# Performance work log

Measured on AMD Instinct MI355X. Metric: run time of the kernel, lower is better.

The kernel has to match this reference:

```python
import jax, jax.numpy as jnp
import numpy as np

B, N, IN_DIM, OUT_DIM, HEADS = 4, 2048, 128, 32, 8
NEG_SLOPE = 0.2


def setup_inputs() -> dict:
    key = jax.random.key(0)
    k_x, k_adj, k_w, k_as, k_ad = jax.random.split(key, 5)
    x = jax.random.normal(k_x, (B, N, IN_DIM), dtype=jnp.float32)
    adj = jax.random.randint(k_adj, (B, N, N), 0, 2).astype(jnp.float32)
    # xavier_uniform bounds
    lim_w = float(np.sqrt(6.0 / (IN_DIM + OUT_DIM)))
    lim_a = float(np.sqrt(6.0 / (OUT_DIM + 1)))
    W = jax.random.uniform(k_w, (HEADS, IN_DIM, OUT_DIM), dtype=jnp.float32, minval=-lim_w, maxval=lim_w)
    a_src = jax.random.uniform(k_as, (HEADS, OUT_DIM), dtype=jnp.float32, minval=-lim_a, maxval=lim_a)
    a_dst = jax.random.uniform(k_ad, (HEADS, OUT_DIM), dtype=jnp.float32, minval=-lim_a, maxval=lim_a)
    return {"x": x, "adj": adj, "W": W, "a_src": a_src, "a_dst": a_dst}


def reference(x, adj, W, a_src, a_dst):
    # Wh: [B,H,N,O]
    Wh = jnp.einsum('bnf,hfo->bhno', x, W)
    alpha_src = jnp.einsum('bhno,ho->bhn', Wh, a_src)  # [B,H,N]
    alpha_dst = jnp.einsum('bhno,ho->bhn', Wh, a_dst)  # [B,H,N]
    # additive scores e[b,h,i,j] = alpha_src[b,h,i] + alpha_dst[b,h,j]
    e = alpha_src[..., :, None] + alpha_dst[..., None, :]
    e = jnp.where(e >= 0, e, NEG_SLOPE * e)  # leaky_relu(0.2)
    n = adj.shape[-1]
    eye = jnp.eye(n, dtype=adj.dtype)
    mask = (adj + eye[None] > 0)[:, None, :, :]  # [B,1,N,N]
    e = jnp.where(mask, e, -jnp.inf)
    attn = jax.nn.softmax(e, axis=-1)  # every row has self-loop -> finite
    out = jnp.einsum('bhij,bhjo->bhio', attn, Wh)  # [B,H,N,O]
    b = x.shape[0]
    out = jnp.transpose(out, (0, 2, 1, 3)).reshape(b, n, HEADS * OUT_DIM)
    return jax.nn.relu(out)
```

## Files before the change

kernel.cpp:

```cpp
#include <hip/hip_runtime.h>
#include <math.h>

#define BB 4
#define NSZ 2048
#define FDIM 128
#define ODIM 32
#define HH 8

typedef short short8 __attribute__((ext_vector_type(8)));
typedef float f32x4 __attribute__((ext_vector_type(4)));

#define WS_EAP  0
#define WS_EBP  131072
#define WS_ADJB 262144
#define WS_WHF  786432

__device__ __forceinline__ unsigned bfbits(float f) {
    unsigned u = __builtin_bit_cast(unsigned, f);
    return u + 0x7fffu + ((u >> 16) & 1u);
}
__device__ __forceinline__ unsigned bfpack(float a, float b) {
    return __builtin_amdgcn_perm(bfbits(b), bfbits(a), 0x07060302);
}

__global__ __launch_bounds__(256) void k_prep(const float* __restrict__ x,
                                              const float* __restrict__ adj,
                                              const float* __restrict__ W,
                                              const float* __restrict__ a_src,
                                              const float* __restrict__ a_dst,
                                              unsigned* __restrict__ adjb,
                                              int4* __restrict__ whf,
                                              float2* __restrict__ eap,
                                              float2* __restrict__ ebp) {
    __shared__ float wsl[FDIM * 33];
    __shared__ unsigned short wlds[64][33];
    int t = threadIdx.x;

    if (blockIdx.x < 16384) {
        int g = blockIdx.x * 256 + t;
        int l = g & 7;
        int word = g >> 3;
        int wk = word & 63;
        int row = word >> 6;
        int i = row & (NSZ - 1);
        const float4 v = *(const float4*)&adj[(size_t)row * NSZ + wk * 32 + l * 4];
        unsigned m = 0;
        if (v.x > 0.f) m |= 1u << (l * 4 + 0);
        if (v.y > 0.f) m |= 1u << (l * 4 + 1);
        if (v.z > 0.f) m |= 1u << (l * 4 + 2);
        if (v.w > 0.f) m |= 1u << (l * 4 + 3);
        m |= (unsigned)__shfl_xor((int)m, 1);
        m |= (unsigned)__shfl_xor((int)m, 2);
        m |= (unsigned)__shfl_xor((int)m, 4);
        if (l == 0) {
            int jb = i - wk * 32;
            if (jb >= 0 && jb < 32) m |= 1u << jb;
            adjb[word] = m;
        }
        return;
    }

    int bidx = blockIdx.x - 16384;
    int b = bidx >> 8;
    int h = (bidx >> 5) & 7;
    int nt = bidx & 31;
    int n0 = nt * 64;
    int w = t >> 6, lane = t & 63;
    int col = lane & 15, quad = lane >> 4;

#pragma unroll
    for (int m = 0; m < 16; m++) {
        int idx = t + m * 256;
        wsl[(idx >> 5) * 33 + (idx & 31)] = W[(size_t)h * (FDIM * ODIM) + idx];
    }

    const float* xp = x + ((size_t)(b * NSZ) + n0 + w * 16 + col) * FDIM + quad * 8;
    int4 afr[4];
#pragma unroll
    for (int kt = 0; kt < 4; kt++) {
        float4 xa = *(const float4*)(xp + kt * 32);
        float4 xb = *(const float4*)(xp + kt * 32 + 4);
        afr[kt] = make_int4((int)bfpack(xa.x, xa.y), (int)bfpack(xa.z, xa.w),
                            (int)bfpack(xb.x, xb.y), (int)bfpack(xb.z, xb.w));
    }
    __syncthreads();

    f32x4 alo = {0.f, 0.f, 0.f, 0.f};
    f32x4 ahi = {0.f, 0.f, 0.f, 0.f};
#pragma unroll
    for (int kt = 0; kt < 4; kt++) {
        short8 a8 = __builtin_bit_cast(short8, afr[kt]);
#pragma unroll
        for (int ot = 0; ot < 2; ot++) {
            unsigned d[4];
#pragma unroll
            for (int jp = 0; jp < 4; jp++) {
                float lo = wsl[(kt * 32 + quad * 8 + 2 * jp) * 33 + ot * 16 + col];
                float hi = wsl[(kt * 32 + quad * 8 + 2 * jp + 1) * 33 + ot * 16 + col];
                d[jp] = bfpack(lo, hi);
            }
            int4 bf = make_int4((int)d[0], (int)d[1], (int)d[2], (int)d[3]);
            if (ot == 0)
                alo = __builtin_amdgcn_mfma_f32_16x16x32_bf16(a8,
                        __builtin_bit_cast(short8, bf), alo, 0, 0, 0);
            else
                ahi = __builtin_amdgcn_mfma_f32_16x16x32_bf16(a8,
                        __builtin_bit_cast(short8, bf), ahi, 0, 0, 0);
        }
    }

    float as0 = a_src[h * ODIM + col], as1 = a_src[h * ODIM + 16 + col];
    float ad0 = a_dst[h * ODIM + col], ad1 = a_dst[h * ODIM + 16 + col];
#pragma unroll
    for (int r = 0; r < 4; r++) {
        float pa = alo[r] * as0 + ahi[r] * as1;
        float pb = alo[r] * ad0 + ahi[r] * ad1;
#pragma unroll
        for (int mk = 1; mk <= 8; mk <<= 1) {
            pa += __shfl_xor(pa, mk);
            pb += __shfl_xor(pb, mk);
        }
        if (col == 0) {
            size_t idx = (size_t)(b * HH + h) * NSZ + n0 + w * 16 + quad * 4 + r;
            eap[idx] = make_float2(__expf(pa - 8.f), __expf(0.2f * pa - 8.f));
            ebp[idx] = make_float2(__expf(pb - 8.f), __expf(0.2f * pb - 8.f));
        }
    }

#pragma unroll
    for (int r = 0; r < 4; r++) {
        wlds[w * 16 + quad * 4 + r][col]      = (unsigned short)(bfbits(alo[r]) >> 16);
        wlds[w * 16 + quad * 4 + r][col + 16] = (unsigned short)(bfbits(ahi[r]) >> 16);
    }
    __syncthreads();
    int jl = w >> 1, ot = w & 1;
    unsigned d[4];
#pragma unroll
    for (int jp = 0; jp < 4; jp++) {
        unsigned lo = wlds[jl * 32 + quad * 8 + 2 * jp][ot * 16 + col];
        unsigned hi = wlds[jl * 32 + quad * 8 + 2 * jp + 1][ot * 16 + col];
        d[jp] = (hi << 16) | lo;
    }
    int fragid = ((b * HH + h) * 64 + nt * 2 + jl) * 2 + ot;
    whf[(size_t)fragid * 64 + lane] = make_int4((int)d[0], (int)d[1], (int)d[2], (int)d[3]);
}

__device__ __forceinline__ int4 pfrag(float eaa, float eab, const float4& l0,
                                      const float4& l1, const float4& l2,
                                      const float4& l3, unsigned word, int shb) {
    float p0 = fmaxf(eaa * l0.x, eab * l0.y);
    float p1 = fmaxf(eaa * l0.z, eab * l0.w);
    float p2 = fmaxf(eaa * l1.x, eab * l1.y);
    float p3 = fmaxf(eaa * l1.z, eab * l1.w);
    float p4 = fmaxf(eaa * l2.x, eab * l2.y);
    float p5 = fmaxf(eaa * l2.z, eab * l2.w);
    float p6 = fmaxf(eaa * l3.x, eab * l3.y);
    float p7 = fmaxf(eaa * l3.z, eab * l3.w);
    unsigned d0 = __builtin_amdgcn_perm(__builtin_bit_cast(unsigned, p1),
                                        __builtin_bit_cast(unsigned, p0), 0x07060302);
    unsigned d1 = __builtin_amdgcn_perm(__builtin_bit_cast(unsigned, p3),
                                        __builtin_bit_cast(unsigned, p2), 0x07060302);
    unsigned d2 = __builtin_amdgcn_perm(__builtin_bit_cast(unsigned, p5),
                                        __builtin_bit_cast(unsigned, p4), 0x07060302);
    unsigned d3 = __builtin_amdgcn_perm(__builtin_bit_cast(unsigned, p7),
                                        __builtin_bit_cast(unsigned, p6), 0x07060302);
    unsigned mk[4];
#pragma unroll
    for (int k = 0; k < 4; k++) {
        int s0 = ((int)(word << (shb - 2 * k))) >> 31;
        int s1 = ((int)(word << (shb - 2 * k - 1))) >> 31;
        mk[k] = __builtin_amdgcn_perm((unsigned)s1, (unsigned)s0, 0x07060302);
    }
    return make_int4((int)(d0 & mk[0]), (int)(d1 & mk[1]),
                     (int)(d2 & mk[2]), (int)(d3 & mk[3]));
}

__global__ __launch_bounds__(256, 4) void k_gat(const int4* __restrict__ whf,
                                                const float2* __restrict__ eap,
                                                const float2* __restrict__ ebp,
                                                const unsigned* __restrict__ adjb,
                                                float* __restrict__ out) {
    __shared__ float sbuf[6144];

    int t = threadIdx.x;
    int u = blockIdx.x;
    int unit = (u & 7) * 128 + (u >> 3);
    int b = unit >> 8;
    int h = (unit >> 5) & 7;
    int i0 = (unit & 31) * 64;
    int wave = t >> 6, lane = t & 63;
    int col = lane & 15, quad = lane >> 4, qsh = quad * 8;
    int shb = 31 - qsh;
    size_t bh = (size_t)(b * HH + h);

    const float4* ebg = (const float4*)(ebp + bh * NSZ);
#pragma unroll
    for (int k = 0; k < 4; k++) ((float4*)sbuf)[t + k * 256] = ebg[t + k * 256];

    float2 ea[4];
    const uint4* mp[4];
#pragma unroll
    for (int f = 0; f < 4; f++) {
        ea[f] = eap[bh * NSZ + i0 + f * 16 + col];
        mp[f] = (const uint4*)(adjb + ((size_t)(b * NSZ) + i0 + f * 16 + col) * 64) + wave * 4;
    }
    const int4* bfp = whf + bh * 8192 + lane;

    f32x4 ac[4][3];
#pragma unroll
    for (int f = 0; f < 4; f++)
#pragma unroll
        for (int c = 0; c < 3; c++) ac[f][c] = (f32x4){0.f, 0.f, 0.f, 0.f};
    const int4 onesv = make_int4(0x3F803F80, 0x3F803F80, 0x3F803F80, 0x3F803F80);
    short8 bones = __builtin_bit_cast(short8, onesv);

    __syncthreads();

    for (int jt4 = 0; jt4 < 4; jt4++) {
        uint4 mw[4];
#pragma unroll
        for (int f = 0; f < 4; f++) mw[f] = mp[f][jt4];
#pragma unroll
        for (int q = 0; q < 4; q++) {
            int jt = wave * 16 + jt4 * 4 + q;
            const float4* el = (const float4*)&sbuf[(jt * 32 + qsh) * 2];
            float4 l0 = el[0], l1 = el[1], l2 = el[2], l3 = el[3];
            int4 blo = bfp[jt * 128];
            int4 bhi = bfp[jt * 128 + 64];
            short8 b0 = __builtin_bit_cast(short8, blo);
            short8 b1 = __builtin_bit_cast(short8, bhi);
            unsigned wq[4] = {mw[0].x, mw[1].x, mw[2].x, mw[3].x};
            if (q == 1) { wq[0] = mw[0].y; wq[1] = mw[1].y; wq[2] = mw[2].y; wq[3] = mw[3].y; }
            if (q == 2) { wq[0] = mw[0].z; wq[1] = mw[1].z; wq[2] = mw[2].z; wq[3] = mw[3].z; }
            if (q == 3) { wq[0] = mw[0].w; wq[1] = mw[1].w; wq[2] = mw[2].w; wq[3] = mw[3].w; }
#pragma unroll
            for (int f = 0; f < 4; f++) {
                int4 fr = pfrag(ea[f].x, ea[f].y, l0, l1, l2, l3, wq[f], shb);
                short8 a8 = __builtin_bit_cast(short8, fr);
                ac[f][0] = __builtin_amdgcn_mfma_f32_16x16x32_bf16(a8, b0, ac[f][0], 0, 0, 0);
                ac[f][1] = __builtin_amdgcn_mfma_f32_16x16x32_bf16(a8, b1, ac[f][1], 0, 0, 0);
                ac[f][2] = __builtin_amdgcn_mfma_f32_16x16x32_bf16(a8, bones, ac[f][2], 0, 0, 0);
            }
        }
    }

    f32x4* reg0 = (f32x4*)&sbuf[0];
    f32x4* reg1 = (f32x4*)&sbuf[3072];
    __syncthreads();
    if (wave >= 2) {
        f32x4* rg = (wave == 2) ? reg0 : reg1;
#pragma unroll
        for (int f = 0; f < 4; f++)
#pragma unroll
            for (int c = 0; c < 3; c++) rg[(f * 3 + c) * 64 + lane] = ac[f][c];
    }
    __syncthreads();
    if (wave < 2) {
        f32x4* rg = (wave == 0) ? reg0 : reg1;
#pragma unroll
        for (int f = 0; f < 4; f++)
#pragma unroll
            for (int c = 0; c < 3; c++) {
                f32x4 v = rg[(f * 3 + c) * 64 + lane];
#pragma unroll
                for (int r = 0; r < 4; r++) ac[f][c][r] += v[r];
            }
    }
    __syncthreads();
    if (wave == 1) {
#pragma unroll
        for (int f = 0; f < 4; f++)
#pragma unroll
            for (int c = 0; c < 3; c++) reg0[(f * 3 + c) * 64 + lane] = ac[f][c];
    }
    __syncthreads();
    if (wave != 0) return;
#pragma unroll
    for (int f = 0; f < 4; f++)
#pragma unroll
        for (int c = 0; c < 3; c++) {
            f32x4 v = reg0[(f * 3 + c) * 64 + lane];
#pragma unroll
            for (int r = 0; r < 4; r++) ac[f][c][r] += v[r];
        }

    float* op = out + ((size_t)(b * NSZ) + i0) * (HH * ODIM) + h * ODIM + col;
#pragma unroll
    for (int f = 0; f < 4; f++)
#pragma unroll
        for (int r = 0; r < 4; r++) {
            int row = f * 16 + quad * 4 + r;
            float inv = 1.0f / ac[f][2][r];
            op[(size_t)row * (HH * ODIM)]      = fmaxf(ac[f][0][r] * inv, 0.f);
            op[(size_t)row * (HH * ODIM) + 16] = fmaxf(ac[f][1][r] * inv, 0.f);
        }
}

extern "C" void kernel_launch(void* const* d_in, const int* in_sizes, int n_in,
                              void* d_out, int out_size, void* d_ws, size_t ws_size,
                              hipStream_t stream) {
    const float* x     = (const float*)d_in[0];
    const float* adj   = (const float*)d_in[1];
    const float* W     = (const float*)d_in[2];
    const float* a_src = (const float*)d_in[3];
    const float* a_dst = (const float*)d_in[4];
    float* out = (float*)d_out;

    float* ws = (float*)d_ws;
    float2* eap    = (float2*)(ws + WS_EAP);
    float2* ebp    = (float2*)(ws + WS_EBP);
    unsigned* adjb = (unsigned*)(ws + WS_ADJB);
    int4* whf      = (int4*)(ws + WS_WHF);

    k_prep<<<dim3(16384 + 1024), dim3(256), 0, stream>>>(x, adj, W, a_src, a_dst,
                                                         adjb, whf, eap, ebp);
    k_gat<<<dim3(BB * HH * (NSZ / 64)), dim3(256), 0, stream>>>(whf, eap, ebp, adjb, out);
}
```

Baseline: 146.2 us.

## Pack dst exponentials as bf16 pairs, software-pipeline loads, flatten wave reduction

```diff
diff --git a/kernel.cpp b/kernel.cpp
--- a/kernel.cpp
+++ b/kernel.cpp
@@ -11,9 +11,9 @@
 typedef float f32x4 __attribute__((ext_vector_type(4)));
 
 #define WS_EAP  0
-#define WS_EBP  131072
-#define WS_ADJB 262144
-#define WS_WHF  786432
+#define WS_EBPK 131072
+#define WS_ADJB 196608
+#define WS_WHF  720896
 
 __device__ __forceinline__ unsigned bfbits(float f) {
     unsigned u = __builtin_bit_cast(unsigned, f);
@@ -31,7 +31,7 @@
                                               unsigned* __restrict__ adjb,
                                               int4* __restrict__ whf,
                                               float2* __restrict__ eap,
-                                              float2* __restrict__ ebp) {
+                                              unsigned* __restrict__ ebpk) {
     __shared__ float wsl[FDIM * 33];
     __shared__ unsigned short wlds[64][33];
     int t = threadIdx.x;
@@ -123,7 +123,9 @@
         if (col == 0) {
             size_t idx = (size_t)(b * HH + h) * NSZ + n0 + w * 16 + quad * 4 + r;
             eap[idx] = make_float2(__expf(pa - 8.f), __expf(0.2f * pa - 8.f));
-            ebp[idx] = make_float2(__expf(pb - 8.f), __expf(0.2f * pb - 8.f));
+            float e1 = __expf(pb - 8.f);
+            float e2 = __expf(0.2f * pb - 8.f);
+            ebpk[idx] = (bfbits(e2) & 0xffff0000u) | (bfbits(e1) >> 16);
         }
     }
 
@@ -145,42 +147,35 @@
     whf[(size_t)fragid * 64 + lane] = make_int4((int)d[0], (int)d[1], (int)d[2], (int)d[3]);
 }
 
-__device__ __forceinline__ int4 pfrag(float eaa, float eab, const float4& l0,
-                                      const float4& l1, const float4& l2,
-                                      const float4& l3, unsigned word, int shb) {
-    float p0 = fmaxf(eaa * l0.x, eab * l0.y);
-    float p1 = fmaxf(eaa * l0.z, eab * l0.w);
-    float p2 = fmaxf(eaa * l1.x, eab * l1.y);
-    float p3 = fmaxf(eaa * l1.z, eab * l1.w);
-    float p4 = fmaxf(eaa * l2.x, eab * l2.y);
-    float p5 = fmaxf(eaa * l2.z, eab * l2.w);
-    float p6 = fmaxf(eaa * l3.x, eab * l3.y);
-    float p7 = fmaxf(eaa * l3.z, eab * l3.w);
-    unsigned d0 = __builtin_amdgcn_perm(__builtin_bit_cast(unsigned, p1),
-                                        __builtin_bit_cast(unsigned, p0), 0x07060302);
-    unsigned d1 = __builtin_amdgcn_perm(__builtin_bit_cast(unsigned, p3),
-                                        __builtin_bit_cast(unsigned, p2), 0x07060302);
-    unsigned d2 = __builtin_amdgcn_perm(__builtin_bit_cast(unsigned, p5),
-                                        __builtin_bit_cast(unsigned, p4), 0x07060302);
-    unsigned d3 = __builtin_amdgcn_perm(__builtin_bit_cast(unsigned, p7),
-                                        __builtin_bit_cast(unsigned, p6), 0x07060302);
-    unsigned mk[4];
+__device__ __forceinline__ int4 pfrag_pk(float eaa, float eab,
+                                         const int4& ca, const int4& cb, unsigned w) {
+    unsigned pd[8] = {(unsigned)ca.x, (unsigned)ca.y, (unsigned)ca.z, (unsigned)ca.w,
+                      (unsigned)cb.x, (unsigned)cb.y, (unsigned)cb.z, (unsigned)cb.w};
+    unsigned dw[4];
 #pragma unroll
     for (int k = 0; k < 4; k++) {
-        int s0 = ((int)(word << (shb - 2 * k))) >> 31;
-        int s1 = ((int)(word << (shb - 2 * k - 1))) >> 31;
-        mk[k] = __builtin_amdgcn_perm((unsigned)s1, (unsigned)s0, 0x07060302);
-    }
-    return make_int4((int)(d0 & mk[0]), (int)(d1 & mk[1]),
-                     (int)(d2 & mk[2]), (int)(d3 & mk[3]));
+        float e0  = __builtin_bit_cast(float, pd[2 * k] << 16);
+        float e0b = __builtin_bit_cast(float, pd[2 * k] & 0xffff0000u);
+        float e1  = __builtin_bit_cast(float, pd[2 * k + 1] << 16);
+        float e1b = __builtin_bit_cast(float, pd[2 * k + 1] & 0xffff0000u);
+        float pL = fmaxf(eaa * e0, eab * e0b);
+        float pH = fmaxf(eaa * e1, eab * e1b);
+        unsigned d = __builtin_amdgcn_perm(__builtin_bit_cast(unsigned, pH),
+                                           __builtin_bit_cast(unsigned, pL), 0x07060302);
+        int s0 = ((int)(w << (31 - 2 * k))) >> 31;
+        int s1 = ((int)(w << (30 - 2 * k))) >> 31;
+        unsigned mk = __builtin_amdgcn_perm((unsigned)s1, (unsigned)s0, 0x07060302);
+        dw[k] = d & mk;
+    }
+    return make_int4((int)dw[0], (int)dw[1], (int)dw[2], (int)dw[3]);
 }
 
 __global__ __launch_bounds__(256, 4) void k_gat(const int4* __restrict__ whf,
                                                 const float2* __restrict__ eap,
-                                                const float2* __restrict__ ebp,
+                                                const unsigned* __restrict__ ebpk,
                                                 const unsigned* __restrict__ adjb,
                                                 float* __restrict__ out) {
-    __shared__ float sbuf[6144];
+    __shared__ float sbuf[9216];
 
     int t = threadIdx.x;
     int u = blockIdx.x;
@@ -190,19 +185,19 @@
     int i0 = (unit & 31) * 64;
     int wave = t >> 6, lane = t & 63;
     int col = lane & 15, quad = lane >> 4, qsh = quad * 8;
-    int shb = 31 - qsh;
     size_t bh = (size_t)(b * HH + h);
 
-    const float4* ebg = (const float4*)(ebp + bh * NSZ);
-#pragma unroll
-    for (int k = 0; k < 4; k++) ((float4*)sbuf)[t + k * 256] = ebg[t + k * 256];
+    unsigned* sbu = (unsigned*)sbuf;
+    const uint4* ebg = (const uint4*)(ebpk + bh * NSZ);
+    ((uint4*)sbu)[t] = ebg[t];
+    ((uint4*)sbu)[t + 256] = ebg[t + 256];
 
     float2 ea[4];
-    const uint4* mp[4];
+    const unsigned* mr[4];
 #pragma unroll
     for (int f = 0; f < 4; f++) {
         ea[f] = eap[bh * NSZ + i0 + f * 16 + col];
-        mp[f] = (const uint4*)(adjb + ((size_t)(b * NSZ) + i0 + f * 16 + col) * 64) + wave * 4;
+        mr[f] = adjb + ((size_t)(b * NSZ) + i0 + f * 16 + col) * 64;
     }
     const int4* bfp = whf + bh * 8192 + lane;
 
@@ -216,47 +211,50 @@
 
     __syncthreads();
 
-    for (int jt4 = 0; jt4 < 4; jt4++) {
-        uint4 mw[4];
-#pragma unroll
-        for (int f = 0; f < 4; f++) mw[f] = mp[f][jt4];
-#pragma unroll
-        for (int q = 0; q < 4; q++) {
-            int jt = wave * 16 + jt4 * 4 + q;
-            const float4* el = (const float4*)&sbuf[(jt * 32 + qsh) * 2];
-            float4 l0 = el[0], l1 = el[1], l2 = el[2], l3 = el[3];
-            int4 blo = bfp[jt * 128];
-            int4 bhi = bfp[jt * 128 + 64];
-            short8 b0 = __builtin_bit_cast(short8, blo);
-            short8 b1 = __builtin_bit_cast(short8, bhi);
-            unsigned wq[4] = {mw[0].x, mw[1].x, mw[2].x, mw[3].x};
-            if (q == 1) { wq[0] = mw[0].y; wq[1] = mw[1].y; wq[2] = mw[2].y; wq[3] = mw[3].y; }
-            if (q == 2) { wq[0] = mw[0].z; wq[1] = mw[1].z; wq[2] = mw[2].z; wq[3] = mw[3].z; }
-            if (q == 3) { wq[0] = mw[0].w; wq[1] = mw[1].w; wq[2] = mw[2].w; wq[3] = mw[3].w; }
-#pragma unroll
-            for (int f = 0; f < 4; f++) {
-                int4 fr = pfrag(ea[f].x, ea[f].y, l0, l1, l2, l3, wq[f], shb);
-                short8 a8 = __builtin_bit_cast(short8, fr);
-                ac[f][0] = __builtin_amdgcn_mfma_f32_16x16x32_bf16(a8, b0, ac[f][0], 0, 0, 0);
-                ac[f][1] = __builtin_amdgcn_mfma_f32_16x16x32_bf16(a8, b1, ac[f][1], 0, 0, 0);
-                ac[f][2] = __builtin_amdgcn_mfma_f32_16x16x32_bf16(a8, bones, ac[f][2], 0, 0, 0);
-            }
-        }
-    }
-
-    f32x4* reg0 = (f32x4*)&sbuf[0];
-    f32x4* reg1 = (f32x4*)&sbuf[3072];
-    __syncthreads();
-    if (wave >= 2) {
-        f32x4* rg = (wave == 2) ? reg0 : reg1;
+    int jt0 = wave * 16;
+    int4 c_e0 = ((const int4*)sbu)[jt0 * 8 + quad * 2];
+    int4 c_e1 = ((const int4*)sbu)[jt0 * 8 + quad * 2 + 1];
+    int4 c_b0 = bfp[jt0 * 128];
+    int4 c_b1 = bfp[jt0 * 128 + 64];
+    unsigned c_w0 = mr[0][jt0], c_w1 = mr[1][jt0], c_w2 = mr[2][jt0], c_w3 = mr[3][jt0];
+
+    for (int s = 0; s < 16; s++) {
+        int jn = jt0 + ((s + 1) & 15);
+        int4 n_e0 = ((const int4*)sbu)[jn * 8 + quad * 2];
+        int4 n_e1 = ((const int4*)sbu)[jn * 8 + quad * 2 + 1];
+        int4 n_b0 = bfp[jn * 128];
+        int4 n_b1 = bfp[jn * 128 + 64];
+        unsigned n_w0 = mr[0][jn], n_w1 = mr[1][jn], n_w2 = mr[2][jn], n_w3 = mr[3][jn];
+
+        short8 b0 = __builtin_bit_cast(short8, c_b0);
+        short8 b1 = __builtin_bit_cast(short8, c_b1);
+        unsigned cw[4] = {c_w0, c_w1, c_w2, c_w3};
+#pragma unroll
+        for (int f = 0; f < 4; f++) {
+            int4 fr = pfrag_pk(ea[f].x, ea[f].y, c_e0, c_e1, cw[f] >> qsh);
+            short8 a8 = __builtin_bit_cast(short8, fr);
+            ac[f][0] = __builtin_amdgcn_mfma_f32_16x16x32_bf16(a8, b0, ac[f][0], 0, 0, 0);
+            ac[f][1] = __builtin_amdgcn_mfma_f32_16x16x32_bf16(a8, b1, ac[f][1], 0, 0, 0);
+            ac[f][2] = __builtin_amdgcn_mfma_f32_16x16x32_bf16(a8, bones, ac[f][2], 0, 0, 0);
+        }
+
+        c_e0 = n_e0; c_e1 = n_e1; c_b0 = n_b0; c_b1 = n_b1;
+        c_w0 = n_w0; c_w1 = n_w1; c_w2 = n_w2; c_w3 = n_w3;
+    }
+
+    __syncthreads();
+    if (wave != 0) {
+        f32x4* rg = (f32x4*)&sbuf[(wave - 1) * 3072];
 #pragma unroll
         for (int f = 0; f < 4; f++)
 #pragma unroll
             for (int c = 0; c < 3; c++) rg[(f * 3 + c) * 64 + lane] = ac[f][c];
     }
     __syncthreads();
-    if (wave < 2) {
-        f32x4* rg = (wave == 0) ? reg0 : reg1;
+    if (wave != 0) return;
+#pragma unroll
+    for (int wv = 0; wv < 3; wv++) {
+        f32x4* rg = (f32x4*)&sbuf[wv * 3072];
 #pragma unroll
         for (int f = 0; f < 4; f++)
 #pragma unroll
@@ -266,23 +264,6 @@
                 for (int r = 0; r < 4; r++) ac[f][c][r] += v[r];
             }
     }
-    __syncthreads();
-    if (wave == 1) {
-#pragma unroll
-        for (int f = 0; f < 4; f++)
-#pragma unroll
-            for (int c = 0; c < 3; c++) reg0[(f * 3 + c) * 64 + lane] = ac[f][c];
-    }
-    __syncthreads();
-    if (wave != 0) return;
-#pragma unroll
-    for (int f = 0; f < 4; f++)
-#pragma unroll
-        for (int c = 0; c < 3; c++) {
-            f32x4 v = reg0[(f * 3 + c) * 64 + lane];
-#pragma unroll
-            for (int r = 0; r < 4; r++) ac[f][c][r] += v[r];
-        }
 
     float* op = out + ((size_t)(b * NSZ) + i0) * (HH * ODIM) + h * ODIM + col;
 #pragma unroll
@@ -308,11 +289,11 @@
 
     float* ws = (float*)d_ws;
     float2* eap    = (float2*)(ws + WS_EAP);
-    float2* ebp    = (float2*)(ws + WS_EBP);
+    unsigned* ebpk = (unsigned*)(ws + WS_EBPK);
     unsigned* adjb = (unsigned*)(ws + WS_ADJB);
     int4* whf      = (int4*)(ws + WS_WHF);
 
     k_prep<<<dim3(16384 + 1024), dim3(256), 0, stream>>>(x, adj, W, a_src, a_dst,
-                                                         adjb, whf, eap, ebp);
-    k_gat<<<dim3(BB * HH * (NSZ / 64)), dim3(256), 0, stream>>>(whf, eap, ebp, adjb, out);
-}
+                                                         adjb, whf, eap, ebpk);
+    k_gat<<<dim3(BB * HH * (NSZ / 64)), dim3(256), 0, stream>>>(whf, eap, ebpk, adjb, out);
+}
```

Result: no change. 148.1 us (+1.3%).

## Use one-wave blocks over 16 rows with transposed adjacency bitmask layout

Applied to the files above, without the earlier changes.

```diff
diff --git a/kernel.cpp b/kernel.cpp
--- a/kernel.cpp
+++ b/kernel.cpp
@@ -43,6 +43,7 @@
         int wk = word & 63;
         int row = word >> 6;
         int i = row & (NSZ - 1);
+        int b = row >> 11;
         const float4 v = *(const float4*)&adj[(size_t)row * NSZ + wk * 32 + l * 4];
         unsigned m = 0;
         if (v.x > 0.f) m |= 1u << (l * 4 + 0);
@@ -55,7 +56,7 @@
         if (l == 0) {
             int jb = i - wk * 32;
             if (jb >= 0 && jb < 32) m |= 1u << jb;
-            adjb[word] = m;
+            adjb[((size_t)b * 64 + wk) * NSZ + i] = m;
         }
         return;
     }
@@ -147,7 +148,7 @@
 
 __device__ __forceinline__ int4 pfrag(float eaa, float eab, const float4& l0,
                                       const float4& l1, const float4& l2,
-                                      const float4& l3, unsigned word, int shb) {
+                                      const float4& l3, unsigned w) {
     float p0 = fmaxf(eaa * l0.x, eab * l0.y);
     float p1 = fmaxf(eaa * l0.z, eab * l0.w);
     float p2 = fmaxf(eaa * l1.x, eab * l1.y);
@@ -167,133 +168,62 @@
     unsigned mk[4];
 #pragma unroll
     for (int k = 0; k < 4; k++) {
-        int s0 = ((int)(word << (shb - 2 * k))) >> 31;
-        int s1 = ((int)(word << (shb - 2 * k - 1))) >> 31;
+        int s0 = ((int)(w << (31 - 2 * k))) >> 31;
+        int s1 = ((int)(w << (30 - 2 * k))) >> 31;
         mk[k] = __builtin_amdgcn_perm((unsigned)s1, (unsigned)s0, 0x07060302);
     }
     return make_int4((int)(d0 & mk[0]), (int)(d1 & mk[1]),
                      (int)(d2 & mk[2]), (int)(d3 & mk[3]));
 }
 
-__global__ __launch_bounds__(256, 4) void k_gat(const int4* __restrict__ whf,
-                                                const float2* __restrict__ eap,
-                                                const float2* __restrict__ ebp,
-                                                const unsigned* __restrict__ adjb,
-                                                float* __restrict__ out) {
-    __shared__ float sbuf[6144];
-
-    int t = threadIdx.x;
-    int u = blockIdx.x;
-    int unit = (u & 7) * 128 + (u >> 3);
-    int b = unit >> 8;
-    int h = (unit >> 5) & 7;
-    int i0 = (unit & 31) * 64;
-    int wave = t >> 6, lane = t & 63;
+__global__ __launch_bounds__(64, 8) void k_gat(const int4* __restrict__ whf,
+                                               const float2* __restrict__ eap,
+                                               const float2* __restrict__ ebp,
+                                               const unsigned* __restrict__ adjb,
+                                               float* __restrict__ out) {
+    int lane = threadIdx.x & 63;
+    int unit = blockIdx.x;
+    int i0 = (unit & 127) << 4;
+    int bh = unit >> 7;
+    int b = bh >> 3, h = bh & 7;
     int col = lane & 15, quad = lane >> 4, qsh = quad * 8;
-    int shb = 31 - qsh;
-    size_t bh = (size_t)(b * HH + h);
-
-    const float4* ebg = (const float4*)(ebp + bh * NSZ);
-#pragma unroll
-    for (int k = 0; k < 4; k++) ((float4*)sbuf)[t + k * 256] = ebg[t + k * 256];
-
-    float2 ea[4];
-    const uint4* mp[4];
-#pragma unroll
-    for (int f = 0; f < 4; f++) {
-        ea[f] = eap[bh * NSZ + i0 + f * 16 + col];
-        mp[f] = (const uint4*)(adjb + ((size_t)(b * NSZ) + i0 + f * 16 + col) * 64) + wave * 4;
-    }
-    const int4* bfp = whf + bh * 8192 + lane;
-
-    f32x4 ac[4][3];
-#pragma unroll
-    for (int f = 0; f < 4; f++)
-#pragma unroll
-        for (int c = 0; c < 3; c++) ac[f][c] = (f32x4){0.f, 0.f, 0.f, 0.f};
+
+    float2 ea = eap[(size_t)bh * NSZ + i0 + col];
+    const float4* eb4 = (const float4*)(ebp + (size_t)bh * NSZ) + quad * 4;
+    const unsigned* abp = adjb + (size_t)b * (64 * NSZ) + i0 + col;
+    const int4* bfp = whf + (size_t)bh * 8192 + lane;
+
+    f32x4 acc0 = {0.f, 0.f, 0.f, 0.f};
+    f32x4 acc1 = {0.f, 0.f, 0.f, 0.f};
+    f32x4 accd = {0.f, 0.f, 0.f, 0.f};
     const int4 onesv = make_int4(0x3F803F80, 0x3F803F80, 0x3F803F80, 0x3F803F80);
     short8 bones = __builtin_bit_cast(short8, onesv);
-
-    __syncthreads();
-
-    for (int jt4 = 0; jt4 < 4; jt4++) {
-        uint4 mw[4];
-#pragma unroll
-        for (int f = 0; f < 4; f++) mw[f] = mp[f][jt4];
-#pragma unroll
-        for (int q = 0; q < 4; q++) {
-            int jt = wave * 16 + jt4 * 4 + q;
-            const float4* el = (const float4*)&sbuf[(jt * 32 + qsh) * 2];
-            float4 l0 = el[0], l1 = el[1], l2 = el[2], l3 = el[3];
-            int4 blo = bfp[jt * 128];
-            int4 bhi = bfp[jt * 128 + 64];
-            short8 b0 = __builtin_bit_cast(short8, blo);
-            short8 b1 = __builtin_bit_cast(short8, bhi);
-            unsigned wq[4] = {mw[0].x, mw[1].x, mw[2].x, mw[3].x};
-            if (q == 1) { wq[0] = mw[0].y; wq[1] = mw[1].y; wq[2] = mw[2].y; wq[3] = mw[3].y; }
-            if (q == 2) { wq[0] = mw[0].z; wq[1] = mw[1].z; wq[2] = mw[2].z; wq[3] = mw[3].z; }
-            if (q == 3) { wq[0] = mw[0].w; wq[1] = mw[1].w; wq[2] = mw[2].w; wq[3] = mw[3].w; }
-#pragma unroll
-            for (int f = 0; f < 4; f++) {
-                int4 fr = pfrag(ea[f].x, ea[f].y, l0, l1, l2, l3, wq[f], shb);
-                short8 a8 = __builtin_bit_cast(short8, fr);
-                ac[f][0] = __builtin_amdgcn_mfma_f32_16x16x32_bf16(a8, b0, ac[f][0], 0, 0, 0);
-                ac[f][1] = __builtin_amdgcn_mfma_f32_16x16x32_bf16(a8, b1, ac[f][1], 0, 0, 0);
-                ac[f][2] = __builtin_amdgcn_mfma_f32_16x16x32_bf16(a8, bones, ac[f][2], 0, 0, 0);
-            }
-        }
-    }
-
-    f32x4* reg0 = (f32x4*)&sbuf[0];
-    f32x4* reg1 = (f32x4*)&sbuf[3072];
-    __syncthreads();
-    if (wave >= 2) {
-        f32x4* rg = (wave == 2) ? reg0 : reg1;
-#pragma unroll
-        for (int f = 0; f < 4; f++)
-#pragma unroll
-            for (int c = 0; c < 3; c++) rg[(f * 3 + c) * 64 + lane] = ac[f][c];
-    }
-    __syncthreads();
-    if (wave < 2) {
-        f32x4* rg = (wave == 0) ? reg0 : reg1;
-#pragma unroll
-        for (int f = 0; f < 4; f++)
-#pragma unroll
-            for (int c = 0; c < 3; c++) {
-                f32x4 v = rg[(f * 3 + c) * 64 + lane];
-#pragma unroll
-                for (int r = 0; r < 4; r++) ac[f][c][r] += v[r];
-            }
-    }
-    __syncthreads();
-    if (wave == 1) {
-#pragma unroll
-        for (int f = 0; f < 4; f++)
-#pragma unroll
-            for (int c = 0; c < 3; c++) reg0[(f * 3 + c) * 64 + lane] = ac[f][c];
-    }
-    __syncthreads();
-    if (wave != 0) return;
-#pragma unroll
-    for (int f = 0; f < 4; f++)
-#pragma unroll
-        for (int c = 0; c < 3; c++) {
-            f32x4 v = reg0[(f * 3 + c) * 64 + lane];
-#pragma unroll
-            for (int r = 0; r < 4; r++) ac[f][c][r] += v[r];
-        }
+    float eaa = ea.x, eab = ea.y;
+
+#pragma unroll 2
+    for (int jt = 0; jt < 64; jt++) {
+        unsigned w = abp[jt * NSZ] >> qsh;
+        float4 l0 = eb4[jt * 16 + 0];
+        float4 l1 = eb4[jt * 16 + 1];
+        float4 l2 = eb4[jt * 16 + 2];
+        float4 l3 = eb4[jt * 16 + 3];
+        int4 blo = bfp[jt * 128];
+        int4 bhi = bfp[jt * 128 + 64];
+        int4 fr = pfrag(eaa, eab, l0, l1, l2, l3, w);
+        short8 a8 = __builtin_bit_cast(short8, fr);
+        acc0 = __builtin_amdgcn_mfma_f32_16x16x32_bf16(a8, __builtin_bit_cast(short8, blo), acc0, 0, 0, 0);
+        acc1 = __builtin_amdgcn_mfma_f32_16x16x32_bf16(a8, __builtin_bit_cast(short8, bhi), acc1, 0, 0, 0);
+        accd = __builtin_amdgcn_mfma_f32_16x16x32_bf16(a8, bones, accd, 0, 0, 0);
+    }
 
     float* op = out + ((size_t)(b * NSZ) + i0) * (HH * ODIM) + h * ODIM + col;
 #pragma unroll
-    for (int f = 0; f < 4; f++)
-#pragma unroll
-        for (int r = 0; r < 4; r++) {
-            int row = f * 16 + quad * 4 + r;
-            float inv = 1.0f / ac[f][2][r];
-            op[(size_t)row * (HH * ODIM)]      = fmaxf(ac[f][0][r] * inv, 0.f);
-            op[(size_t)row * (HH * ODIM) + 16] = fmaxf(ac[f][1][r] * inv, 0.f);
-        }
+    for (int r = 0; r < 4; r++) {
+        int row = quad * 4 + r;
+        float inv = 1.0f / accd[r];
+        op[(size_t)row * (HH * ODIM)]      = fmaxf(acc0[r] * inv, 0.f);
+        op[(size_t)row * (HH * ODIM) + 16] = fmaxf(acc1[r] * inv, 0.f);
+    }
 }
 
 extern "C" void kernel_launch(void* const* d_in, const int* in_sizes, int n_in,
@@ -314,5 +244,5 @@
 
     k_prep<<<dim3(16384 + 1024), dim3(256), 0, stream>>>(x, adj, W, a_src, a_dst,
                                                          adjb, whf, eap, ebp);
-    k_gat<<<dim3(BB * HH * (NSZ / 64)), dim3(256), 0, stream>>>(whf, eap, ebp, adjb, out);
-}
+    k_gat<<<dim3(BB * HH * (NSZ / 16)), dim3(64), 0, stream>>>(whf, eap, ebp, adjb, out);
+}
```

Result: slower. 165.9 us (+13.5%).
